# Performance work log

Hardware: AMD Instinct MI355X
Metric: run time of the kernel (lower is better)

Reference implementation:

```python
import jax, jax.numpy as jnp
import numpy as np

B, P, C, NO = 64, 16384, 81, 32
THRESHOLD = 0.5
NEG_POS_RATIO = 3
ALPHA = 1.0


def cxcy_to_xy(c):
    return jnp.concatenate([c[:, :2] - c[:, 2:] / 2, c[:, :2] + c[:, 2:] / 2], axis=1)


def xy_to_cxcy(x):
    return jnp.concatenate([(x[:, :2] + x[:, 2:]) / 2, x[:, 2:] - x[:, :2]], axis=1)


def cxcy_to_gcxgcy(cxcy, priors_cxcy):
    # SSD encoding: offsets scaled by 10, log-size scaled by 5
    g_cxcy = (cxcy[:, :2] - priors_cxcy[:, :2]) / (priors_cxcy[:, 2:] / 10.0)
    g_wh = jnp.log(cxcy[:, 2:] / priors_cxcy[:, 2:]) * 5.0
    return jnp.concatenate([g_cxcy, g_wh], axis=1)


def jaccard(a, b):
    # a: [N,4] xy, b: [M,4] xy -> IoU [N,M]
    lo = jnp.maximum(a[:, None, :2], b[None, :, :2])
    hi = jnp.minimum(a[:, None, 2:], b[None, :, 2:])
    wh = jnp.clip(hi - lo, 0.0)
    inter = wh[..., 0] * wh[..., 1]
    area_a = (a[:, 2] - a[:, 0]) * (a[:, 3] - a[:, 1])
    area_b = (b[:, 2] - b[:, 0]) * (b[:, 3] - b[:, 1])
    union = area_a[:, None] + area_b[None, :] - inter
    return inter / union


def setup_inputs() -> dict:
    key = jax.random.key(0)
    k1, k2, k3, k4, k5, k6 = jax.random.split(key, 6)
    predicted_locs = jax.random.normal(k1, (B, P, 4), dtype=jnp.float32)
    predicted_scores = jax.random.normal(k2, (B, P, C), dtype=jnp.float32)
    # valid boxes in [0,1] with xmax>xmin, ymax>ymin
    corners = jax.random.uniform(k3, (B, NO, 2, 2), dtype=jnp.float32)
    lo = jnp.min(corners, axis=2)
    hi = jnp.max(corners, axis=2)
    hi = jnp.minimum(jnp.maximum(hi, lo + 0.02), 1.0)
    boxes = jnp.concatenate([lo, hi], axis=-1)
    labels = jax.random.randint(k4, (B, NO), 1, C, dtype=jnp.int32)
    prior_cc = jax.random.uniform(k5, (P, 2), minval=0.1, maxval=0.9, dtype=jnp.float32)
    prior_wh = jax.random.uniform(k6, (P, 2), minval=0.05, maxval=0.4, dtype=jnp.float32)
    priors_cxcy = jnp.concatenate([prior_cc, prior_wh], axis=1)
    return {"predicted_locs": predicted_locs, "predicted_scores": predicted_scores,
            "boxes": boxes, "labels": labels, "priors_cxcy": priors_cxcy}


def reference(predicted_locs, predicted_scores, boxes, labels, priors_cxcy):
    priors_xy = cxcy_to_xy(priors_cxcy)

    def match(bx, lb):
        ov = jaccard(bx, priors_xy)                       # [NO, P]
        ov_for_prior = jnp.max(ov, axis=0)                # [P]
        obj_for_prior = jnp.argmax(ov, axis=0)            # [P]
        prior_for_obj = jnp.argmax(ov, axis=1)            # [NO]
        # force every object to own its best prior
        obj_for_prior = obj_for_prior.at[prior_for_obj].set(jnp.arange(NO))
        ov_for_prior = ov_for_prior.at[prior_for_obj].set(1.0)
        lab = lb[obj_for_prior]
        lab = jnp.where(ov_for_prior < THRESHOLD, 0, lab)
        true_locs = cxcy_to_gcxgcy(xy_to_cxcy(bx[obj_for_prior]), priors_cxcy)
        return true_locs, lab

    true_locs, true_classes = jax.vmap(match)(boxes, labels)  # [B,P,4], [B,P]

    pos = true_classes != 0                               # [B,P]
    n_pos = jnp.sum(pos, axis=1)                          # [B]
    total_pos = jnp.sum(n_pos).astype(jnp.float32)

    # L1 loss (mean over positive prior elements)
    loc_abs = jnp.abs(predicted_locs - true_locs)
    loc_loss = jnp.sum(loc_abs * pos[..., None].astype(loc_abs.dtype)) / (total_pos * 4.0)

    # per-anchor cross entropy
    logp = jax.nn.log_softmax(predicted_scores, axis=-1)
    ce = -jnp.take_along_axis(logp, true_classes[..., None], axis=-1)[..., 0]  # [B,P]

    conf_pos_sum = jnp.sum(ce * pos.astype(ce.dtype))
    ce_neg = jnp.where(pos, 0.0, ce)
    ce_neg_sorted = -jnp.sort(-ce_neg, axis=1)            # descending
    hard = jnp.arange(P)[None, :] < (NEG_POS_RATIO * n_pos)[:, None]
    conf_neg_sum = jnp.sum(ce_neg_sorted * hard.astype(ce.dtype))

    conf_loss = (conf_pos_sum + conf_neg_sum) / total_pos
    return conf_loss + ALPHA * loc_loss
```

## Files before the change

### kernel.cpp

```cpp
#include <hip/hip_runtime.h>
#include <hip/hip_bf16.h>
#include <cstdint>
#include <cstddef>

#define BB 64
#define PP 16384
#define CC 81
#define NOBJ 32

typedef float f4u __attribute__((ext_vector_type(4), aligned(4)));


__global__ __launch_bounds__(256) void argmax_init_kernel(
        const float* __restrict__ boxes,
        const float* __restrict__ priors,
        int* __restrict__ pfo,
        int* __restrict__ n_pos,
        double* __restrict__ acc,
        int* __restrict__ done) {
    int o = blockIdx.x;
    int b = blockIdx.y;
    int tid = threadIdx.x;

    if (o == 0 && b == 0) {
        if (tid < BB) n_pos[tid] = 0;
        if (tid >= 64 && tid < 67) acc[tid - 64] = 0.0;
        if (tid == 67) *done = 0;
    }

    float4 bx = ((const float4*)boxes)[b * NOBJ + o];
    float a0 = bx.x, a1 = bx.y, a2 = bx.z, a3 = bx.w;
    float areaA = (a2 - a0) * (a3 - a1);

    float bestv = -1.f;
    int besti = 0;
    for (int i = 0; i < PP / 256; ++i) {
        int p = i * 256 + tid;
        float4 pc = ((const float4*)priors)[p];
        float px1 = pc.x - pc.z * 0.5f, py1 = pc.y - pc.w * 0.5f;
        float px2 = pc.x + pc.z * 0.5f, py2 = pc.y + pc.w * 0.5f;
        float lx = fmaxf(a0, px1), ly = fmaxf(a1, py1);
        float hx = fminf(a2, px2), hy = fminf(a3, py2);
        float iw = fmaxf(hx - lx, 0.f), ih = fmaxf(hy - ly, 0.f);
        float inter = iw * ih;
        float areaB = (px2 - px1) * (py2 - py1);
        float v = inter / (areaA + areaB - inter);
        if (v > bestv) { bestv = v; besti = p; }
    }
    for (int off = 32; off; off >>= 1) {
        float v2 = __shfl_down(bestv, off);
        int   i2 = __shfl_down(besti, off);
        if (v2 > bestv || (v2 == bestv && i2 < besti)) { bestv = v2; besti = i2; }
    }
    __shared__ float sV[4];
    __shared__ int   sI[4];
    int lane = tid & 63, wid = tid >> 6;
    if (lane == 0) { sV[wid] = bestv; sI[wid] = besti; }
    __syncthreads();
    if (tid == 0) {
        float v = sV[0]; int ix = sI[0];
        for (int w = 1; w < 4; ++w) {
            if (sV[w] > v || (sV[w] == v && sI[w] < ix)) { v = sV[w]; ix = sI[w]; }
        }
        pfo[b * NOBJ + o] = ix;
    }
}

__global__ __launch_bounds__(256, 8) void matchce_kernel(
        const float* __restrict__ predicted_locs,
        const float* __restrict__ scores,
        const float* __restrict__ boxes,
        const int* __restrict__ labels,
        const float* __restrict__ priors,
        const int* __restrict__ pfo,
        int* __restrict__ n_pos,
        double* __restrict__ partial_loc,
        double* __restrict__ partial_pos,
        float* __restrict__ ce_neg) {
    __shared__ float sB[NOBJ * 4];
    __shared__ int sL[NOBJ];
    __shared__ int sP[NOBJ];
    __shared__ float sLs[4];
    __shared__ int sCs[4];

    int b = blockIdx.y;
    int tid = threadIdx.x;
    int p = blockIdx.x * 256 + tid;
    if (tid < NOBJ * 4) sB[tid] = boxes[b * NOBJ * 4 + tid];
    if (tid < NOBJ) { sL[tid] = labels[b * NOBJ + tid]; sP[tid] = pfo[b * NOBJ + tid]; }
    __syncthreads();

    float4 pc = ((const float4*)priors)[p];
    float px1 = pc.x - pc.z * 0.5f, py1 = pc.y - pc.w * 0.5f;
    float px2 = pc.x + pc.z * 0.5f, py2 = pc.y + pc.w * 0.5f;

    float bestv = -1.f; int besto = 0;
#pragma unroll
    for (int o = 0; o < NOBJ; ++o) {
        float lx = fmaxf(sB[o * 4], px1), ly = fmaxf(sB[o * 4 + 1], py1);
        float hx = fminf(sB[o * 4 + 2], px2), hy = fminf(sB[o * 4 + 3], py2);
        float iw = fmaxf(hx - lx, 0.f), ih = fmaxf(hy - ly, 0.f);
        float inter = iw * ih;
        float areaA = (sB[o * 4 + 2] - sB[o * 4]) * (sB[o * 4 + 3] - sB[o * 4 + 1]);
        float areaB = (px2 - px1) * (py2 - py1);
        float v = inter / (areaA + areaB - inter);
        if (v > bestv) { bestv = v; besto = o; }
    }
#pragma unroll
    for (int o = NOBJ - 1; o >= 0; --o) {
        if (sP[o] == p) { besto = o; bestv = 1.0f; break; }
    }
    int lab = (bestv < 0.5f) ? 0 : sL[besto];

    float l1 = 0.f;
    bool pos = (lab != 0);
    if (pos) {
        float bx0 = sB[besto * 4], bx1 = sB[besto * 4 + 1];
        float bx2 = sB[besto * 4 + 2], bx3 = sB[besto * 4 + 3];
        float cx = (bx0 + bx2) * 0.5f, cy = (bx1 + bx3) * 0.5f;
        float w = bx2 - bx0, h = bx3 - bx1;
        float g0 = (cx - pc.x) / (pc.z / 10.0f);
        float g1 = (cy - pc.y) / (pc.w / 10.0f);
        float g2 = __logf(w / pc.z) * 5.0f;
        float g3 = __logf(h / pc.w) * 5.0f;
        float4 pl = ((const float4*)predicted_locs)[(size_t)b * PP + p];
        l1 = fabsf(pl.x - g0) + fabsf(pl.y - g1) + fabsf(pl.z - g2) + fabsf(pl.w - g3);
    }

    int lane = tid & 63, wv = tid >> 6;
    float l1r = l1;
    for (int off = 32; off; off >>= 1) l1r += __shfl_down(l1r, off);
    unsigned long long bal = __ballot(pos);
    if (lane == 0) { sLs[wv] = l1r; sCs[wv] = __popcll(bal); }
    __syncthreads();
    if (tid == 0) {
        float Lr = sLs[0] + sLs[1] + sLs[2] + sLs[3];
        int cnt = sCs[0] + sCs[1] + sCs[2] + sCs[3];
        partial_loc[b * 64 + blockIdx.x] = (double)Lr;
        if (cnt) atomicAdd(&n_pos[b], cnt);
    }

    int q = lane >> 2, r = lane & 3;
    int brow = blockIdx.x * 256 + wv * 64;
    double accpos = 0.0;

#pragma unroll
    for (int pp = 0; pp < 4; ++pp) {
        int lr = pp * 16 + q;
        int prow = brow + lr;
        size_t row = (size_t)b * PP + prow;
        const float* rp = scores + row * CC;
        const float* rpl = rp + 4 * r;

        f4u w0, w1, w2, w3, w4;
        float w80;
        asm volatile(
            "global_load_dwordx4 %0, %6, off\n\t"
            "global_load_dwordx4 %1, %6, off offset:64\n\t"
            "global_load_dwordx4 %2, %6, off offset:128\n\t"
            "global_load_dwordx4 %3, %6, off offset:192\n\t"
            "global_load_dwordx4 %4, %6, off offset:256\n\t"
            "global_load_dword %5, %7, off offset:320\n\t"
            "s_waitcnt vmcnt(0)"
            : "=&v"(w0), "=&v"(w1), "=&v"(w2), "=&v"(w3), "=&v"(w4), "=&v"(w80)
            : "v"(rpl), "v"(rp));

        int lab_r = __shfl(lab, lr);
        float slab = rp[lab_r];

        float e0 = __expf(w0.x) + __expf(w1.x) + __expf(w2.x) + __expf(w3.x) + __expf(w4.x);
        float e1 = __expf(w0.y) + __expf(w1.y) + __expf(w2.y) + __expf(w3.y) + __expf(w4.y);
        float e2 = __expf(w0.z) + __expf(w1.z) + __expf(w2.z) + __expf(w3.z) + __expf(w4.z);
        float e3 = __expf(w0.w) + __expf(w1.w) + __expf(w2.w) + __expf(w3.w) + __expf(w4.w);
        float e = (e0 + e1) + (e2 + e3);
        if (r == 0) e += __expf(w80);

        e += __shfl_xor(e, 1);
        e += __shfl_xor(e, 2);

        float cev = __logf(e) - slab;
        if (r == 0) {
            bool posr = (lab_r != 0);
            ce_neg[row] = posr ? 0.f : cev;
            if (posr) accpos += (double)cev;
        }
    }
    for (int off = 32; off; off >>= 1) accpos += __shfl_down(accpos, off);
    if (lane == 0)
        partial_pos[((size_t)b * 64 + blockIdx.x) * 4 + wv] = accpos;
}

__global__ __launch_bounds__(512, 1) void mine_final_kernel(
        const float* __restrict__ ce_neg,
        const int* __restrict__ n_pos,
        const double* __restrict__ partial_loc,
        const double* __restrict__ partial_pos,
        double* __restrict__ batch_res,
        int* __restrict__ done,
        float* __restrict__ out) {
    int b = blockIdx.x;
    int tid = threadIdx.x;
    int lane = tid & 63, wid = tid >> 6;
    const float* row = ce_neg + (size_t)b * PP;

    float vals[32];
#pragma unroll
    for (int i = 0; i < 32; ++i) vals[i] = row[tid + i * 512];

    double sp = (tid < 256) ? partial_pos[b * 256 + tid] : 0.0;
    double sl = (tid < 64) ? partial_loc[b * 64 + tid] : 0.0;
    __shared__ double sD[8], sE[8];
    for (int off = 32; off; off >>= 1) {
        sp += __shfl_down(sp, off);
        sl += __shfl_down(sl, off);
    }
    if (lane == 0) { sD[wid] = sp; sE[wid] = sl; }

    int K = 3 * n_pos[b];
    if (K > PP) K = PP;
    __shared__ int sC[8];
    __shared__ float sS[8];

    double cn = 0.0;
    if (K > 0) {
        unsigned lo = 0u, hi = 0xFFFFFFFFu;
        while (lo < hi) {
            unsigned mid = (unsigned)(((unsigned long long)lo + (unsigned long long)hi + 1ull) >> 1);
            int c = 0;
#pragma unroll
            for (int i = 0; i < 32; ++i) c += (__float_as_uint(vals[i]) >= mid) ? 1 : 0;
            for (int off = 32; off; off >>= 1) c += __shfl_down(c, off);
            if (lane == 0) sC[wid] = c;
            __syncthreads();
            int ctot = sC[0] + sC[1] + sC[2] + sC[3] + sC[4] + sC[5] + sC[6] + sC[7];
            __syncthreads();
            if (ctot >= K) lo = mid; else hi = mid - 1;
        }
        float x = __uint_as_float(lo);
        int cgt = 0; float sgt = 0.f;
#pragma unroll
        for (int i = 0; i < 32; ++i) {
            if (__float_as_uint(vals[i]) > lo) { cgt++; sgt += vals[i]; }
        }
        for (int off = 32; off; off >>= 1) {
            cgt += __shfl_down(cgt, off);
            sgt += __shfl_down(sgt, off);
        }
        if (lane == 0) { sC[wid] = cgt; sS[wid] = sgt; }
        __syncthreads();
        if (tid == 0) {
            int cg = sC[0] + sC[1] + sC[2] + sC[3] + sC[4] + sC[5] + sC[6] + sC[7];
            float sg = sS[0] + sS[1] + sS[2] + sS[3] + sS[4] + sS[5] + sS[6] + sS[7];
            cn = (double)sg + (double)(K - cg) * (double)x;
        }
    } else {
        __syncthreads();
    }

    if (tid == 0) {
        double cp = sD[0] + sD[1] + sD[2] + sD[3] + sD[4] + sD[5] + sD[6] + sD[7];
        double lc = sE[0] + sE[1] + sE[2] + sE[3] + sE[4] + sE[5] + sE[6] + sE[7];
        batch_res[b * 4 + 0] = cp;
        batch_res[b * 4 + 1] = lc;
        batch_res[b * 4 + 2] = cn;
        batch_res[b * 4 + 3] = (double)n_pos[b];
    }

    __threadfence();
    __shared__ int ticket;
    if (tid == 0) ticket = atomicAdd(done, 1);
    __syncthreads();
    if (ticket == BB - 1) {
        double cp = 0.0, lc = 0.0, cn2 = 0.0, np = 0.0;
        if (tid < BB) {
            cp  = batch_res[tid * 4 + 0];
            lc  = batch_res[tid * 4 + 1];
            cn2 = batch_res[tid * 4 + 2];
            np  = batch_res[tid * 4 + 3];
        }
        for (int off = 32; off; off >>= 1) {
            cp += __shfl_down(cp, off);
            lc += __shfl_down(lc, off);
            cn2 += __shfl_down(cn2, off);
            np += __shfl_down(np, off);
        }
        if (tid == 0) {
            double tp = np;
            out[0] = (float)((cp + cn2) / tp + lc / (tp * 4.0));
        }
    }
}

extern "C" void kernel_launch(void* const* d_in, const int* in_sizes, int n_in,
                              void* d_out, int out_size, void* d_ws, size_t ws_size,
                              hipStream_t stream) {
    const float* predicted_locs = (const float*)d_in[0];
    const float* scores         = (const float*)d_in[1];
    const float* boxes          = (const float*)d_in[2];
    const int*   labels         = (const int*)d_in[3];
    const float* priors         = (const float*)d_in[4];
    float* out = (float*)d_out;

    char* ws = (char*)d_ws;
    int*    pfo         = (int*)(ws + 0);
    int*    n_pos       = (int*)(ws + 8192);
    double* acc         = (double*)(ws + 8448);
    int*    done        = (int*)(ws + 8472);
    double* partial_loc = (double*)(ws + 8480);
    double* batch_res   = (double*)(ws + 41248);
    double* partial_pos = (double*)(ws + 49152);
    float*  ce_neg      = (float*)(ws + 196608);

    hipLaunchKernelGGL(argmax_init_kernel, dim3(NOBJ, BB), dim3(256), 0, stream,
                       boxes, priors, pfo, n_pos, acc, done);
    hipLaunchKernelGGL(matchce_kernel, dim3(PP / 256, BB), dim3(256), 0, stream,
                       predicted_locs, scores, boxes, labels, priors, pfo,
                       n_pos, partial_loc, partial_pos, ce_neg);
    hipLaunchKernelGGL(mine_final_kernel, dim3(BB), dim3(512), 0, stream,
                       ce_neg, n_pos, partial_loc, partial_pos, batch_res, done, out);
}
```

Before: 162.4 us.

## Double-buffer score row loads and pick label logit from registers

Restructures the cross-entropy loop in the match kernel so each wave issues the score loads for the next row group before computing on the current one. It uses two register buffers with partial vmcnt waits and sched barriers to overlap memory latency with the exp and log work. Each row is now read with six aligned 16-byte loads and masking, which also lets the label's logit be taken from registers instead of an extra dependent global load. The extra registers lead to lowering the occupancy hint from 8 to 4 blocks per CU, and a redundant else-branch barrier is dropped from the final kernel.

```diff
diff --git a/kernel.cpp b/kernel.cpp
--- a/kernel.cpp
+++ b/kernel.cpp
@@ -9,6 +9,59 @@
 #define NOBJ 32
 
 typedef float f4u __attribute__((ext_vector_type(4), aligned(4)));
+
+#define SB0() __builtin_amdgcn_sched_barrier(0)
+
+#define ISSUE6(P, W0, W1, W2, W3, W4, W5)                               \
+    asm volatile(                                                       \
+        "global_load_dwordx4 %0, %6, off\n\t"                           \
+        "global_load_dwordx4 %1, %6, off offset:64\n\t"                 \
+        "global_load_dwordx4 %2, %6, off offset:128\n\t"                \
+        "global_load_dwordx4 %3, %6, off offset:192\n\t"                \
+        "global_load_dwordx4 %4, %6, off offset:256\n\t"                \
+        "global_load_dwordx4 %5, %6, off offset:320"                    \
+        : "=&v"(W0), "=&v"(W1), "=&v"(W2), "=&v"(W3), "=&v"(W4),        \
+          "=&v"(W5)                                                     \
+        : "v"(P));                                                      \
+    SB0()
+
+#define VMWAIT(N)                                                      \
+    asm volatile("s_waitcnt vmcnt(" #N ")");                            \
+    SB0()
+
+#define PICK4(W, j) (((j) & 2) ? (((j) & 1) ? (W).w : (W).z)            \
+                               : (((j) & 1) ? (W).y : (W).x))
+
+#define ACCC(W, K)                                                     \
+    { int t0 = 4 * rl - q + 16 * (K);                                   \
+      e0 += ((unsigned)(t0 + 0) < 81u) ? __expf((W).x) : 0.f;           \
+      e1 += ((unsigned)(t0 + 1) < 81u) ? __expf((W).y) : 0.f;           \
+      e2 += ((unsigned)(t0 + 2) < 81u) ? __expf((W).z) : 0.f;           \
+      e3 += ((unsigned)(t0 + 3) < 81u) ? __expf((W).w) : 0.f; }
+
+#define CE_COMPUTE(W0, W1, W2, W3, W4, W5, PPI, CEV, LABR)              \
+    {                                                                   \
+        int lr_ = (PPI) * 16 + q;                                       \
+        int lab_r = __shfl(lab, lr_);                                   \
+        LABR = lab_r;                                                   \
+        float e0 = 0.f, e1 = 0.f, e2 = 0.f, e3 = 0.f;                   \
+        ACCC(W0, 0) ACCC(W1, 1) ACCC(W2, 2)                             \
+        ACCC(W3, 3) ACCC(W4, 4) ACCC(W5, 5)                             \
+        float e = (e0 + e1) + (e2 + e3);                                \
+        int wlab = q + lab_r;                   \
+        int j_ = wlab & 3;                                              \
+        int k_ = wlab >> 4;                                             \
+        int own_ = (wlab >> 2) & 3;                                     \
+        float c0_ = PICK4(W0, j_), c1_ = PICK4(W1, j_);                 \
+        float c2_ = PICK4(W2, j_), c3_ = PICK4(W3, j_);                 \
+        float c4_ = PICK4(W4, j_), c5_ = PICK4(W5, j_);                 \
+        float cc_ = (k_ == 0) ? c0_ : (k_ == 1) ? c1_ : (k_ == 2) ? c2_ \
+                  : (k_ == 3) ? c3_ : (k_ == 4) ? c4_ : c5_;            \
+        float sb_ = (own_ == rl) ? cc_ : 0.f;                           \
+        e  += __shfl_xor(e, 1);   e  += __shfl_xor(e, 2);               \
+        sb_ += __shfl_xor(sb_, 1); sb_ += __shfl_xor(sb_, 2);           \
+        CEV = __logf(e) - sb_;                                          \
+    }
 
 
 __global__ __launch_bounds__(256) void argmax_init_kernel(
@@ -66,7 +119,7 @@
     }
 }
 
-__global__ __launch_bounds__(256, 8) void matchce_kernel(
+__global__ __launch_bounds__(256, 4) void matchce_kernel(
         const float* __restrict__ predicted_locs,
         const float* __restrict__ scores,
         const float* __restrict__ boxes,
@@ -140,50 +193,47 @@
         if (cnt) atomicAdd(&n_pos[b], cnt);
     }
 
-    int q = lane >> 2, r = lane & 3;
-    int brow = blockIdx.x * 256 + wv * 64;
+    int q = lane >> 2, rl = lane & 3;
+    size_t rowbase = (size_t)b * PP + blockIdx.x * 256 + wv * 64;
+
+    const float* rp0 = scores + (rowbase + 0  + q) * CC;
+    const float* rp1 = scores + (rowbase + 16 + q) * CC;
+    const float* rp2 = scores + (rowbase + 32 + q) * CC;
+    const float* rp3 = scores + (rowbase + 48 + q) * CC;
+    const float* pl0 = (rp0 - q) + 4 * rl;
+    const float* pl1 = (rp1 - q) + 4 * rl;
+    const float* pl2 = (rp2 - q) + 4 * rl;
+    const float* pl3 = (rp3 - q) + 4 * rl;
+
+    f4u A0, A1, A2, A3, A4, A5;
+    f4u B0, B1, B2, B3, B4, B5;
+    float cev0, cev1, cev2, cev3;
+    int lb0, lb1, lb2, lb3;
+
+    ISSUE6(pl0, A0, A1, A2, A3, A4, A5);
+    ISSUE6(pl1, B0, B1, B2, B3, B4, B5);
+    VMWAIT(6);
+    CE_COMPUTE(A0, A1, A2, A3, A4, A5, 0, cev0, lb0);
+    ISSUE6(pl2, A0, A1, A2, A3, A4, A5);
+    VMWAIT(6);
+    CE_COMPUTE(B0, B1, B2, B3, B4, B5, 1, cev1, lb1);
+    ISSUE6(pl3, B0, B1, B2, B3, B4, B5);
+    VMWAIT(6);
+    CE_COMPUTE(A0, A1, A2, A3, A4, A5, 2, cev2, lb2);
+    VMWAIT(0);
+    CE_COMPUTE(B0, B1, B2, B3, B4, B5, 3, cev3, lb3);
+
     double accpos = 0.0;
-
-#pragma unroll
-    for (int pp = 0; pp < 4; ++pp) {
-        int lr = pp * 16 + q;
-        int prow = brow + lr;
-        size_t row = (size_t)b * PP + prow;
-        const float* rp = scores + row * CC;
-        const float* rpl = rp + 4 * r;
-
-        f4u w0, w1, w2, w3, w4;
-        float w80;
-        asm volatile(
-            "global_load_dwordx4 %0, %6, off\n\t"
-            "global_load_dwordx4 %1, %6, off offset:64\n\t"
-            "global_load_dwordx4 %2, %6, off offset:128\n\t"
-            "global_load_dwordx4 %3, %6, off offset:192\n\t"
-            "global_load_dwordx4 %4, %6, off offset:256\n\t"
-            "global_load_dword %5, %7, off offset:320\n\t"
-            "s_waitcnt vmcnt(0)"
-            : "=&v"(w0), "=&v"(w1), "=&v"(w2), "=&v"(w3), "=&v"(w4), "=&v"(w80)
-            : "v"(rpl), "v"(rp));
-
-        int lab_r = __shfl(lab, lr);
-        float slab = rp[lab_r];
-
-        float e0 = __expf(w0.x) + __expf(w1.x) + __expf(w2.x) + __expf(w3.x) + __expf(w4.x);
-        float e1 = __expf(w0.y) + __expf(w1.y) + __expf(w2.y) + __expf(w3.y) + __expf(w4.y);
-        float e2 = __expf(w0.z) + __expf(w1.z) + __expf(w2.z) + __expf(w3.z) + __expf(w4.z);
-        float e3 = __expf(w0.w) + __expf(w1.w) + __expf(w2.w) + __expf(w3.w) + __expf(w4.w);
-        float e = (e0 + e1) + (e2 + e3);
-        if (r == 0) e += __expf(w80);
-
-        e += __shfl_xor(e, 1);
-        e += __shfl_xor(e, 2);
-
-        float cev = __logf(e) - slab;
-        if (r == 0) {
-            bool posr = (lab_r != 0);
-            ce_neg[row] = posr ? 0.f : cev;
-            if (posr) accpos += (double)cev;
-        }
+    if (rl == 0) {
+        bool p0_ = (lb0 != 0), p1_ = (lb1 != 0), p2_ = (lb2 != 0), p3_ = (lb3 != 0);
+        ce_neg[rowbase + 0  + q] = p0_ ? 0.f : cev0;
+        ce_neg[rowbase + 16 + q] = p1_ ? 0.f : cev1;
+        ce_neg[rowbase + 32 + q] = p2_ ? 0.f : cev2;
+        ce_neg[rowbase + 48 + q] = p3_ ? 0.f : cev3;
+        if (p0_) accpos += (double)cev0;
+        if (p1_) accpos += (double)cev1;
+        if (p2_) accpos += (double)cev2;
+        if (p3_) accpos += (double)cev3;
     }
     for (int off = 32; off; off >>= 1) accpos += __shfl_down(accpos, off);
     if (lane == 0)
@@ -253,8 +303,6 @@
             float sg = sS[0] + sS[1] + sS[2] + sS[3] + sS[4] + sS[5] + sS[6] + sS[7];
             cn = (double)sg + (double)(K - cg) * (double)x;
         }
-    } else {
-        __syncthreads();
     }
 
     if (tid == 0) {
```

Result: faster. 144.4 us, median of 3 (-11.1%).
